# Optimization experiments

Measured on AMD Instinct MI355X. Metric: run time of the kernel, lower is better.

## Reference

```python
import jax, jax.numpy as jnp
import numpy as np

N, L, E, H, D = 4, 2048, 1024, 16, 64

def setup_inputs() -> dict:
    key = jax.random.key(0)
    ks = jax.random.split(key, 8)
    s = 1.0 / np.sqrt(E)
    return {
        "Q": jax.random.normal(ks[0], (N, L, E), jnp.float32),
        "K": jax.random.normal(ks[1], (N, L, E), jnp.float32),
        "V": jax.random.normal(ks[2], (N, L, E), jnp.float32),
        "Wq": jax.random.normal(ks[3], (H * D, E), jnp.float32) * s,
        "bq": jnp.zeros((H * D,), jnp.float32),
        "Wk": jax.random.normal(ks[4], (H * D, E), jnp.float32) * s,
        "bk": jnp.zeros((H * D,), jnp.float32),
        "Wv": jax.random.normal(ks[5], (H * D, E), jnp.float32) * s,
        "bv": jnp.zeros((H * D,), jnp.float32),
        "Wo": jax.random.normal(ks[6], (E, H * D), jnp.float32) * s,
        "bo": jnp.zeros((E,), jnp.float32),
    }

def reference(Q, K, V, Wq, bq, Wk, bk, Wv, bv, Wo, bo):
    n, lq, e = Q.shape
    lk = K.shape[1]
    # projections: Linear(x) = x @ W.T + b
    q = (Q @ Wq.T + bq).reshape(n, lq, H, D)
    k = (K @ Wk.T + bk).reshape(n, lk, H, D)
    v = (V @ Wv.T + bv).reshape(n, lk, H, D)
    # scores over key dim (original broadcasts Q*K and sums over d)
    scores = jnp.einsum('nqhd,nkhd->nqkh', q, k) / jnp.sqrt(jnp.float32(D))
    attn = jax.nn.softmax(scores, axis=2)  # softmax over key axis
    out = jnp.einsum('nqkh,nkhd->nqhd', attn, v)
    out = out.reshape(n, lq, H * D)
    return (out @ Wo.T + bo).reshape(n, lq, E)
```

## Files before the change

### kernel.cpp

```cpp
#include <hip/hip_runtime.h>
#include <cstdint>
#include <cstddef>


typedef __bf16 bf16x8 __attribute__((ext_vector_type(8)));
typedef __bf16 bf16x4 __attribute__((ext_vector_type(4)));
typedef float f32x4 __attribute__((ext_vector_type(4)));
typedef _Float16 half4v __attribute__((ext_vector_type(4)));

#define LOG2E_OVER_SQRTD 0.18033688011112042f

__device__ __forceinline__ unsigned short f2bf(float f) {
  unsigned int u = __builtin_bit_cast(unsigned int, f);
  u = (u + 0x7fffu + ((u >> 16) & 1u)) >> 16;
  return (unsigned short)u;
}

__device__ __forceinline__ void gl2lds16(const void* g, void* l) {
  __builtin_amdgcn_global_load_lds(
      (__attribute__((address_space(1))) unsigned int*)g,
      (__attribute__((address_space(3))) unsigned int*)l, 16, 0, 0);
}

struct CvtAll {
  const float* src[7];
  unsigned short* dst[7];
};
__global__ __launch_bounds__(256) void cvt_all_k(CvtAll a) {
  int bid = blockIdx.x;
  int slot, local;
  if (bid < 24576) {
    slot = bid >> 13;
    local = bid & 8191;
  } else {
    int w = bid - 24576;
    slot = 3 + (w >> 10);
    local = w & 1023;
  }
  size_t i = ((size_t)local * 256 + threadIdx.x) * 4;
  float4 v = *(const float4*)(a.src[slot] + i);
  ushort4 o;
  o.x = f2bf(v.x); o.y = f2bf(v.y); o.z = f2bf(v.z); o.w = f2bf(v.w);
  *(ushort4*)(a.dst[slot] + i) = o;
}

struct GemmDesc {
  const unsigned short* A;
  const unsigned short* Bt;
  const float* bias;
  void* C;
  int N;
  int nbx_shift;
  float scale;
  int bias_row;
  int out_mode;
};
struct GemmPack3 {
  GemmDesc g[3];
};

__global__ __launch_bounds__(256, 2) void gemm_multi_k(GemmPack3 p) {
  __shared__ __attribute__((aligned(16))) unsigned short As[128 * 64];
  __shared__ __attribute__((aligned(16))) unsigned short Bs[128 * 64];
  const GemmDesc d = p.g[blockIdx.x >> 9];
  const int t = blockIdx.x & 511;
  const int bx = t & ((1 << d.nbx_shift) - 1);
  const int by = t >> d.nbx_shift;

  const int tid = threadIdx.x;
  const int lane = tid & 63, wave = tid >> 6;
  const int lr = lane & 15, lg = lane >> 4;
  const int rowBase = by * 128;
  const int colBase = bx * 128;
  const int wm = (wave & 1) * 64, wn = (wave >> 1) * 64;

  f32x4 acc[4][4] = {};

  const unsigned short* gA[4];
  const unsigned short* gB[4];
  unsigned short* lA[4];
  unsigned short* lB[4];
#pragma unroll
  for (int i = 0; i < 4; ++i) {
    int s = tid + i * 256;
    int row = s >> 3;
    int c = (s & 7) ^ (row & 7);
    gA[i] = d.A + (size_t)(rowBase + row) * 1024 + c * 8;
    gB[i] = d.Bt + (size_t)(colBase + row) * 1024 + c * 8;
    lA[i] = &As[s * 8];
    lB[i] = &Bs[s * 8];
  }

  for (int kt = 0; kt < 16; ++kt) {
    const int ko = kt * 64;
#pragma unroll
    for (int i = 0; i < 4; ++i) {
      gl2lds16(gA[i] + ko, lA[i]);
      gl2lds16(gB[i] + ko, lB[i]);
    }
    __syncthreads();

#pragma unroll
    for (int ks = 0; ks < 2; ++ks) {
      bf16x8 af[4], bfr[4];
#pragma unroll
      for (int mt = 0; mt < 4; ++mt) {
        int row = wm + mt * 16 + lr;
        int c = (ks * 4 + lg) ^ (row & 7);
        af[mt] = *(const bf16x8*)&As[row * 64 + c * 8];
      }
#pragma unroll
      for (int nt = 0; nt < 4; ++nt) {
        int row = wn + nt * 16 + lr;
        int c = (ks * 4 + lg) ^ (row & 7);
        bfr[nt] = *(const bf16x8*)&Bs[row * 64 + c * 8];
      }
#pragma unroll
      for (int mt = 0; mt < 4; ++mt)
#pragma unroll
        for (int nt = 0; nt < 4; ++nt)
          acc[mt][nt] = __builtin_amdgcn_mfma_f32_16x16x32_bf16(
              af[mt], bfr[nt], acc[mt][nt], 0, 0, 0);
    }
    __syncthreads();
  }

#pragma unroll
  for (int mt = 0; mt < 4; ++mt)
#pragma unroll
    for (int nt = 0; nt < 4; ++nt) {
      int col = colBase + wn + nt * 16 + lr;
      float bcol = d.bias_row ? 0.f : d.bias[col];
#pragma unroll
      for (int r = 0; r < 4; ++r) {
        int row = rowBase + wm + mt * 16 + lg * 4 + r;
        float b = d.bias_row ? d.bias[row] : bcol;
        float val = (acc[mt][nt][r] + b) * d.scale;
        size_t idx = (size_t)row * (size_t)d.N + (size_t)col;
        if (d.out_mode == 0)
          ((float*)d.C)[idx] = val;
        else if (d.out_mode == 1)
          ((unsigned short*)d.C)[idx] = f2bf(val);
        else
          ((unsigned short*)d.C)[idx] =
              __builtin_bit_cast(unsigned short, (_Float16)val);
      }
    }
}

__global__ __launch_bounds__(256, 2) void attn_k(
    const unsigned short* __restrict__ qb,
    const unsigned short* __restrict__ kb,
    const unsigned short* __restrict__ vtb,
    unsigned short* __restrict__ aob) {
  __shared__ __attribute__((aligned(16))) unsigned short Ks[2][64 * 64];
  __shared__ __attribute__((aligned(16))) unsigned short Vts[2][64 * 64];

  const int tid = threadIdx.x;
  const int lane = tid & 63, wave = tid >> 6;
  const int lr = lane & 15, lg = lane >> 4;

  const int bid = blockIdx.x;
  const int qt = bid & 7;
  const int nh = bid >> 3;
  const int h = nh & 15, n = nh >> 4;
  const int q0 = qt * 256;
  const int qw = q0 + wave * 64;

  bf16x8 b_q[4][2];
#pragma unroll
  for (int nt = 0; nt < 4; ++nt)
#pragma unroll
    for (int ks = 0; ks < 2; ++ks) {
      size_t tok = (size_t)n * 2048 + qw + nt * 16 + lr;
      b_q[nt][ks] =
          *(const bf16x8*)(qb + (tok << 10) + h * 64 + ks * 32 + lg * 8);
    }

#pragma unroll
  for (int i = 0; i < 2; ++i) {
    int s = i * 256 + tid;
    int row = s >> 3;
    int c = (s & 7) ^ (row & 7);
    gl2lds16(kb + (((size_t)n * 2048 + row) << 10) + h * 64 + c * 8,
             &Ks[0][s * 8]);
    gl2lds16(vtb + (((size_t)(h * 64 + row)) << 13) + (size_t)n * 2048 + c * 8,
             &Vts[0][s * 8]);
  }
  __syncthreads();

  f32x4 o_acc[4][4] = {};
  f32x4 lrow = {0.f, 0.f, 0.f, 0.f};

  for (int kt = 0; kt < 32; ++kt) {
    const int cur = kt & 1;
    if (kt < 31) {
      const int k0 = (kt + 1) * 64;
#pragma unroll
      for (int i = 0; i < 2; ++i) {
        int s = i * 256 + tid;
        int row = s >> 3;
        int c = (s & 7) ^ (row & 7);
        gl2lds16(kb + (((size_t)n * 2048 + k0 + row) << 10) + h * 64 + c * 8,
                 &Ks[cur ^ 1][s * 8]);
        gl2lds16(vtb + (((size_t)(h * 64 + row)) << 13) + (size_t)n * 2048 +
                     k0 + c * 8,
                 &Vts[cur ^ 1][s * 8]);
      }
    }

    half4v pfrag[4][4];
#pragma unroll
    for (int mt = 0; mt < 4; ++mt) {
      bf16x8 a_k[2];
#pragma unroll
      for (int ks = 0; ks < 2; ++ks) {
        int row = mt * 16 + lr;
        int c = (ks * 4 + lg) ^ (row & 7);
        a_k[ks] = *(const bf16x8*)&Ks[cur][row * 64 + c * 8];
      }
#pragma unroll
      for (int nt = 0; nt < 4; ++nt) {
        f32x4 s = {0.f, 0.f, 0.f, 0.f};
        s = __builtin_amdgcn_mfma_f32_16x16x32_bf16(a_k[0], b_q[nt][0], s, 0,
                                                    0, 0);
        s = __builtin_amdgcn_mfma_f32_16x16x32_bf16(a_k[1], b_q[nt][1], s, 0,
                                                    0, 0);
        f32x4 pv;
#pragma unroll
        for (int r = 0; r < 4; ++r) pv[r] = __builtin_amdgcn_exp2f(s[r]);
        lrow[nt] += (pv[0] + pv[1]) + (pv[2] + pv[3]);
        pfrag[mt][nt] = __builtin_convertvector(pv, half4v);
      }
    }

#pragma unroll
    for (int kc = 0; kc < 4; ++kc) {
      half4v a_v[4];
#pragma unroll
      for (int mt = 0; mt < 4; ++mt) {
        int row = mt * 16 + lr;
        int keyoff = kc * 16 + lg * 4;
        int c = (keyoff >> 3) ^ (row & 7);
        a_v[mt] = *(const half4v*)&Vts[cur][row * 64 + c * 8 + (keyoff & 7)];
      }
#pragma unroll
      for (int mt = 0; mt < 4; ++mt)
#pragma unroll
        for (int nt = 0; nt < 4; ++nt)
          o_acc[mt][nt] = __builtin_amdgcn_mfma_f32_16x16x16f16(
              a_v[mt], pfrag[kc][nt], o_acc[mt][nt], 0, 0, 0);
    }

    __syncthreads();
  }

  float inv[4];
#pragma unroll
  for (int nt = 0; nt < 4; ++nt) {
    float l = lrow[nt];
    l += __shfl_xor(l, 16);
    l += __shfl_xor(l, 32);
    inv[nt] = 1.0f / l;
  }
#pragma unroll
  for (int nt = 0; nt < 4; ++nt) {
    size_t tok = (size_t)n * 2048 + qw + nt * 16 + lr;
#pragma unroll
    for (int mt = 0; mt < 4; ++mt) {
      f32x4 ov = o_acc[mt][nt] * inv[nt];
      bf16x4 o4 = __builtin_convertvector(ov, bf16x4);
      uint2 od = __builtin_bit_cast(uint2, o4);
      *(uint2*)(aob + (tok << 10) + h * 64 + mt * 16 + lg * 4) = od;
    }
  }
}

extern "C" void kernel_launch(void* const* d_in, const int* in_sizes, int n_in,
                              void* d_out, int out_size, void* d_ws,
                              size_t ws_size, hipStream_t stream) {
  const float* Q = (const float*)d_in[0];
  const float* K = (const float*)d_in[1];
  const float* V = (const float*)d_in[2];
  const float* Wq = (const float*)d_in[3];
  const float* bq = (const float*)d_in[4];
  const float* Wk = (const float*)d_in[5];
  const float* bk = (const float*)d_in[6];
  const float* Wv = (const float*)d_in[7];
  const float* bv = (const float*)d_in[8];
  const float* Wo = (const float*)d_in[9];
  const float* bo = (const float*)d_in[10];

  const size_t S = (size_t)8192 * 1024;
  const size_t W = (size_t)1024 * 1024;
  unsigned short* ws = (unsigned short*)d_ws;
  unsigned short* Qbf = ws;
  unsigned short* Kbf = ws + S;
  unsigned short* Vbf = ws + 2 * S;
  unsigned short* qbuf = ws + 3 * S;
  unsigned short* kbuf = ws + 4 * S;
  unsigned short* vtbuf = ws + 5 * S;
  unsigned short* Wqb = ws + 6 * S;
  unsigned short* Wkb = Wqb + W;
  unsigned short* Wvb = Wqb + 2 * W;
  unsigned short* Wob = Wqb + 3 * W;
  unsigned short* aob = Qbf;

  CvtAll ca;
  ca.src[0] = Q;  ca.dst[0] = Qbf;
  ca.src[1] = K;  ca.dst[1] = Kbf;
  ca.src[2] = V;  ca.dst[2] = Vbf;
  ca.src[3] = Wq; ca.dst[3] = Wqb;
  ca.src[4] = Wk; ca.dst[4] = Wkb;
  ca.src[5] = Wv; ca.dst[5] = Wvb;
  ca.src[6] = Wo; ca.dst[6] = Wob;
  cvt_all_k<<<28672, 256, 0, stream>>>(ca);

  GemmPack3 pp;
  pp.g[0] = {Qbf, Wqb, bq, qbuf, 1024, 3, LOG2E_OVER_SQRTD, 0, 1};
  pp.g[1] = {Kbf, Wkb, bk, kbuf, 1024, 3, 1.0f, 0, 1};
  pp.g[2] = {Wvb, Vbf, bv, vtbuf, 8192, 6, 1.0f, 1, 2};
  gemm_multi_k<<<1536, 256, 0, stream>>>(pp);

  attn_k<<<512, 256, 0, stream>>>(qbuf, kbuf, vtbuf, aob);

  GemmPack3 po;
  po.g[0] = {aob, Wob, bo, d_out, 1024, 3, 1.0f, 0, 0};
  po.g[1] = po.g[0];
  po.g[2] = po.g[0];
  gemm_multi_k<<<512, 256, 0, stream>>>(po);
}
```

Measured before the change: 353.3 us.

## Split attention over two key halves with a combine kernel and raise occupancy

The attention kernel now splits the 2048 keys into two halves, one per block. This doubles the grid to 1024 blocks and halves each block's serial key loop. Each half writes its unnormalized bf16 output and per-row sums to workspace, and a new combine kernel adds the halves and normalizes. This is valid because the kernel uses no running max. The launch-bound occupancy hints rise to 4 for attention and 3 for the GEMM. That risks register spills and adds an extra memory pass for the partial outputs.

New measurement: 686.1 us. 94.2% more time.

```diff
diff --git a/kernel.cpp b/kernel.cpp
--- a/kernel.cpp
+++ b/kernel.cpp
@@ -6,6 +6,7 @@
 typedef __bf16 bf16x8 __attribute__((ext_vector_type(8)));
 typedef __bf16 bf16x4 __attribute__((ext_vector_type(4)));
 typedef float f32x4 __attribute__((ext_vector_type(4)));
+typedef float f32x8 __attribute__((ext_vector_type(8)));
 typedef _Float16 half4v __attribute__((ext_vector_type(4)));
 
 #define LOG2E_OVER_SQRTD 0.18033688011112042f
@@ -59,7 +60,7 @@
   GemmDesc g[3];
 };
 
-__global__ __launch_bounds__(256, 2) void gemm_multi_k(GemmPack3 p) {
+__global__ __launch_bounds__(256, 3) void gemm_multi_k(GemmPack3 p) {
   __shared__ __attribute__((aligned(16))) unsigned short As[128 * 64];
   __shared__ __attribute__((aligned(16))) unsigned short Bs[128 * 64];
   const GemmDesc d = p.g[blockIdx.x >> 9];
@@ -148,11 +149,12 @@
     }
 }
 
-__global__ __launch_bounds__(256, 2) void attn_k(
+__global__ __launch_bounds__(256, 4) void attn_k(
     const unsigned short* __restrict__ qb,
     const unsigned short* __restrict__ kb,
     const unsigned short* __restrict__ vtb,
-    unsigned short* __restrict__ aob) {
+    unsigned short* __restrict__ op,
+    float* __restrict__ lp) {
   __shared__ __attribute__((aligned(16))) unsigned short Ks[2][64 * 64];
   __shared__ __attribute__((aligned(16))) unsigned short Vts[2][64 * 64];
 
@@ -161,11 +163,13 @@
   const int lr = lane & 15, lg = lane >> 4;
 
   const int bid = blockIdx.x;
-  const int qt = bid & 7;
-  const int nh = bid >> 3;
+  const int kh = bid & 1;
+  const int qt = (bid >> 1) & 7;
+  const int nh = bid >> 4;
   const int h = nh & 15, n = nh >> 4;
   const int q0 = qt * 256;
   const int qw = q0 + wave * 64;
+  const int kbase = kh * 1024;
 
   bf16x8 b_q[4][2];
 #pragma unroll
@@ -182,9 +186,10 @@
     int s = i * 256 + tid;
     int row = s >> 3;
     int c = (s & 7) ^ (row & 7);
-    gl2lds16(kb + (((size_t)n * 2048 + row) << 10) + h * 64 + c * 8,
+    gl2lds16(kb + (((size_t)n * 2048 + kbase + row) << 10) + h * 64 + c * 8,
              &Ks[0][s * 8]);
-    gl2lds16(vtb + (((size_t)(h * 64 + row)) << 13) + (size_t)n * 2048 + c * 8,
+    gl2lds16(vtb + (((size_t)(h * 64 + row)) << 13) + (size_t)n * 2048 + kbase +
+                 c * 8,
              &Vts[0][s * 8]);
   }
   __syncthreads();
@@ -192,10 +197,10 @@
   f32x4 o_acc[4][4] = {};
   f32x4 lrow = {0.f, 0.f, 0.f, 0.f};
 
-  for (int kt = 0; kt < 32; ++kt) {
+  for (int kt = 0; kt < 16; ++kt) {
     const int cur = kt & 1;
-    if (kt < 31) {
-      const int k0 = (kt + 1) * 64;
+    if (kt < 15) {
+      const int k0 = kbase + (kt + 1) * 64;
 #pragma unroll
       for (int i = 0; i < 2; ++i) {
         int s = i * 256 + tid;
@@ -255,25 +260,48 @@
     __syncthreads();
   }
 
-  float inv[4];
 #pragma unroll
   for (int nt = 0; nt < 4; ++nt) {
     float l = lrow[nt];
     l += __shfl_xor(l, 16);
     l += __shfl_xor(l, 32);
-    inv[nt] = 1.0f / l;
-  }
-#pragma unroll
-  for (int nt = 0; nt < 4; ++nt) {
     size_t tok = (size_t)n * 2048 + qw + nt * 16 + lr;
+    if (lg == 0) lp[(size_t)kh * (8192 * 16) + tok * 16 + h] = l;
 #pragma unroll
     for (int mt = 0; mt < 4; ++mt) {
-      f32x4 ov = o_acc[mt][nt] * inv[nt];
-      bf16x4 o4 = __builtin_convertvector(ov, bf16x4);
+      bf16x4 o4 = __builtin_convertvector(o_acc[mt][nt], bf16x4);
       uint2 od = __builtin_bit_cast(uint2, o4);
-      *(uint2*)(aob + (tok << 10) + h * 64 + mt * 16 + lg * 4) = od;
-    }
-  }
+      *(uint2*)(op + (size_t)kh * (8192 * 1024) + (tok << 10) + h * 64 +
+                mt * 16 + lg * 4) = od;
+    }
+  }
+}
+
+__global__ __launch_bounds__(256) void combine_k(
+    const unsigned short* __restrict__ op, const float* __restrict__ lp,
+    unsigned short* __restrict__ aob) {
+  const size_t S = (size_t)8192 * 1024;
+  size_t idx = ((size_t)blockIdx.x * 256 + threadIdx.x) * 8;
+  int tok = (int)(idx >> 10);
+  int h = (int)((idx & 1023) >> 6);
+  float la = lp[(size_t)tok * 16 + h];
+  float lb = lp[(size_t)8192 * 16 + (size_t)tok * 16 + h];
+  float inv = 1.0f / (la + lb);
+  bf16x8 a = *(const bf16x8*)(op + idx);
+  bf16x8 b = *(const bf16x8*)(op + S + idx);
+  f32x8 fa = __builtin_convertvector(a, f32x8);
+  f32x8 fb = __builtin_convertvector(b, f32x8);
+  ushort4 o0, o1;
+  o0.x = f2bf((fa[0] + fb[0]) * inv);
+  o0.y = f2bf((fa[1] + fb[1]) * inv);
+  o0.z = f2bf((fa[2] + fb[2]) * inv);
+  o0.w = f2bf((fa[3] + fb[3]) * inv);
+  o1.x = f2bf((fa[4] + fb[4]) * inv);
+  o1.y = f2bf((fa[5] + fb[5]) * inv);
+  o1.z = f2bf((fa[6] + fb[6]) * inv);
+  o1.w = f2bf((fa[7] + fb[7]) * inv);
+  *(ushort4*)(aob + idx) = o0;
+  *(ushort4*)(aob + idx + 4) = o1;
 }
 
 extern "C" void kernel_launch(void* const* d_in, const int* in_sizes, int n_in,
@@ -304,7 +332,9 @@
   unsigned short* Wkb = Wqb + W;
   unsigned short* Wvb = Wqb + 2 * W;
   unsigned short* Wob = Wqb + 3 * W;
-  unsigned short* aob = Qbf;
+  unsigned short* op = ws;
+  float* lp = (float*)(ws + 2 * S);
+  unsigned short* aob = qbuf;
 
   CvtAll ca;
   ca.src[0] = Q;  ca.dst[0] = Qbf;
@@ -322,7 +352,8 @@
   pp.g[2] = {Wvb, Vbf, bv, vtbuf, 8192, 6, 1.0f, 1, 2};
   gemm_multi_k<<<1536, 256, 0, stream>>>(pp);
 
-  attn_k<<<512, 256, 0, stream>>>(qbuf, kbuf, vtbuf, aob);
+  attn_k<<<1024, 256, 0, stream>>>(qbuf, kbuf, vtbuf, op, lp);
+  combine_k<<<4096, 256, 0, stream>>>(op, lp, aob);
 
   GemmPack3 po;
   po.g[0] = {aob, Wob, bo, d_out, 1024, 3, 1.0f, 0, 0};
```
